# Kernel tuning notes

Hardware: AMD Instinct MI355X
Metric: run time of the kernel (lower is better)

The kernel has to match this reference:

```python
import jax, jax.numpy as jnp
import numpy as np

D_MODEL = 2048
NUM_HEADS = 32
NUM_GROUPS = 8
HEAD_DIM = D_MODEL // NUM_HEADS  # 64
HPG = NUM_HEADS // NUM_GROUPS    # heads per group = 4
B, S = 2, 2048


def setup_inputs() -> dict:
    key = jax.random.key(0)
    ks = jax.random.split(key, 11)
    sd = 1.0 / np.sqrt(D_MODEL)
    kv_dim = HEAD_DIM * NUM_GROUPS
    return {
        "q": jax.random.normal(ks[0], (B, S, D_MODEL), jnp.float32),
        "k": jax.random.normal(ks[1], (B, S, D_MODEL), jnp.float32),
        "v": jax.random.normal(ks[2], (B, S, D_MODEL), jnp.float32),
        "Wq": jax.random.normal(ks[3], (D_MODEL, D_MODEL), jnp.float32) * sd,
        "bq": jnp.zeros((D_MODEL,), jnp.float32),
        "Wk": jax.random.normal(ks[4], (D_MODEL, kv_dim), jnp.float32) * sd,
        "bk": jnp.zeros((kv_dim,), jnp.float32),
        "Wv": jax.random.normal(ks[5], (D_MODEL, kv_dim), jnp.float32) * sd,
        "bv": jnp.zeros((kv_dim,), jnp.float32),
        "Wo": jax.random.normal(ks[6], (D_MODEL, D_MODEL), jnp.float32) * sd,
        "bo": jnp.zeros((D_MODEL,), jnp.float32),
    }


def reference(q, k, v, Wq, bq, Wk, bk, Wv, bv, Wo, bo):
    b, qlen, _ = q.shape
    kvlen = k.shape[1]
    # projections
    qh = (q @ Wq + bq).reshape(b, qlen, NUM_GROUPS, HPG, HEAD_DIM)   # [b,s,g,h,d]
    kh = (k @ Wk + bk).reshape(b, kvlen, NUM_GROUPS, HEAD_DIM)        # [b,t,g,d]
    vh = (v @ Wv + bv).reshape(b, kvlen, NUM_GROUPS, HEAD_DIM)        # [b,t,g,d]
    scale = 1.0 / np.sqrt(HEAD_DIM).astype(np.float32)
    # grouped attention: each group's heads share the same K/V
    scores = jnp.einsum('bsghd,btgd->bghst', qh, kh) * scale          # [b,g,h,s,t]
    attn = jax.nn.softmax(scores, axis=-1)                            # dropout = identity (eval)
    out = jnp.einsum('bghst,btgd->bsghd', attn, vh)                   # [b,s,g,h,d]
    out = out.reshape(b, qlen, D_MODEL)
    return out @ Wo + bo
```

## Files before the change

kernel.cpp:

```cpp
#include <hip/hip_runtime.h>

typedef unsigned short u16;
typedef unsigned int u32;
typedef __attribute__((ext_vector_type(8))) short bf16x8;
typedef __attribute__((ext_vector_type(4))) float f32x4;
typedef __attribute__((ext_vector_type(16))) float f32x16;

#define DM 2048
#define SQ_SCALE (0.125f * 1.44269504089f)

__device__ __forceinline__ u16 f2bf(float f) {
  union { float f; u32 u; } v; v.f = f;
  u32 r = v.u + 0x7fffu + ((v.u >> 16) & 1u);
  return (u16)(r >> 16);
}
__device__ __forceinline__ u32 pkrn(float lo, float hi) {
  union { float f; u32 u; } a, b; a.f = lo; b.f = hi;
  return ((a.u + 0x8000u) >> 16) | ((b.u + 0x8000u) & 0xffff0000u);
}
__device__ __forceinline__ u32 cvtpk(float lo, float hi) {
  u32 r;
  asm("v_cvt_pk_bf16_f32 %0, %1, %2" : "=v"(r) : "v"(lo), "v"(hi));
  return r;
}
__device__ __forceinline__ void gload16(const u16* g, u16* l) {
  __builtin_amdgcn_global_load_lds((const __attribute__((address_space(1))) void*)g,
                                   (__attribute__((address_space(3))) void*)l, 16, 0, 0);
}

__global__ __launch_bounds__(256) void prep(const float* __restrict__ q,
                                            const float* __restrict__ k,
                                            const float* __restrict__ v,
                                            const float* __restrict__ Wq,
                                            const float* __restrict__ Wk,
                                            const float* __restrict__ Wv,
                                            const float* __restrict__ Wo,
                                            u16* __restrict__ qb,
                                            u16* __restrict__ kb,
                                            u16* __restrict__ vb,
                                            u16* __restrict__ WqkvT,
                                            u16* __restrict__ WoT) {
  __shared__ u16 s[64][72];
  int bid = blockIdx.x;
  if (bid < 12288) {
    int z = bid >> 12, x = bid & 4095;
    const float* in = (z == 0) ? q : (z == 1) ? k : v;
    u16* out = (z == 0) ? qb : (z == 1) ? kb : vb;
    size_t i = ((size_t)x * 256 + threadIdx.x) * 8;
    float4 f0 = *(const float4*)(in + i);
    float4 f1 = *(const float4*)(in + i + 4);
    uint4 w = {pkrn(f0.x, f0.y), pkrn(f0.z, f0.w), pkrn(f1.x, f1.y), pkrn(f1.z, f1.w)};
    *(uint4*)(out + i) = w;
    return;
  }
  int off = bid - 12288;
  const float* in; u16* out; int K, N, bx, by;
  if (off < 1024)      { in = Wq; out = WqkvT;                          K = 2048; N = 2048; bx = off & 31; by = off >> 5; }
  else if (off < 1280) { int i2 = off - 1024; in = Wk; out = WqkvT + (size_t)2048 * 2048; K = 2048; N = 512; bx = i2 & 7; by = i2 >> 3; }
  else if (off < 1536) { int i2 = off - 1280; in = Wv; out = WqkvT + (size_t)2560 * 2048; K = 2048; N = 512; bx = i2 & 7; by = i2 >> 3; }
  else                 { int i2 = off - 1536; in = Wo; out = WoT;       K = 2048; N = 2048; bx = i2 & 31; by = i2 >> 5; }
  int n0 = bx * 64, k0 = by * 64;
  int t = threadIdx.x;
  int r = t >> 2;
  int cc = (t & 3) * 16;
  const float* ip = in + (size_t)(k0 + r) * N + n0 + cc;
  u16 tmp[16];
#pragma unroll
  for (int i = 0; i < 16; i += 4) {
    float4 vv = *(const float4*)(ip + i);
    tmp[i] = f2bf(vv.x); tmp[i + 1] = f2bf(vv.y);
    tmp[i + 2] = f2bf(vv.z); tmp[i + 3] = f2bf(vv.w);
  }
  *(uint4*)&s[r][cc] = *(uint4*)tmp;
  *(uint4*)&s[r][cc + 8] = *(uint4*)(tmp + 8);
  __syncthreads();
#pragma unroll
  for (int i = 0; i < 16; i++) tmp[i] = s[cc + i][r];
  u16* op = out + (size_t)(n0 + r) * K + k0 + cc;
  *(uint4*)op = *(uint4*)tmp;
  *(uint4*)(op + 8) = *(uint4*)(tmp + 8);
}

__global__ __launch_bounds__(256) void gemm_proj(const u16* __restrict__ qb,
                                                 const u16* __restrict__ kb,
                                                 const u16* __restrict__ vb,
                                                 const u16* __restrict__ Bt,
                                                 const float* __restrict__ bqp,
                                                 const float* __restrict__ bkp,
                                                 const float* __restrict__ bvp,
                                                 u16* __restrict__ qhb,
                                                 u16* __restrict__ kvb,
                                                 u16* __restrict__ vtb) {
  __shared__ u16 As[2][128 * 32];
  __shared__ u16 Bs[2][128 * 32];
  int n0 = blockIdx.x * 128, m0 = blockIdx.y * 128;
  const u16* A; const float* bias; u16* C; int cw, bofs; float esc;
  if (n0 < 2048)      { A = qb; bias = bqp; C = qhb; cw = 2048; bofs = 0;    esc = SQ_SCALE; }
  else if (n0 < 2560) { A = kb; bias = bkp; C = kvb; cw = 1024; bofs = 2048; esc = 1.0f; }
  else                { A = vb; bias = bvp; C = kvb; cw = 1024; bofs = 2560; esc = 1.0f; }
  int ccol0 = (n0 < 2048) ? n0 : (n0 - 2048);

  int tid = threadIdx.x, wave = tid >> 6, lane = tid & 63;
  int lq = lane & 15, quad = lane >> 4;
  int wm = (wave & 1) * 64, wn = (wave >> 1) * 64;

  f32x4 zero = {0.f, 0.f, 0.f, 0.f};
  f32x4 acc[4][4];
#pragma unroll
  for (int i = 0; i < 4; i++)
#pragma unroll
    for (int j = 0; j < 4; j++) acc[i][j] = zero;

  const u16* gA = A + (size_t)(m0 + wave * 16 + (lane >> 2)) * 2048 + (lane & 3) * 8;
  const u16* gB = Bt + (size_t)(n0 + wave * 16 + (lane >> 2)) * 2048 + (lane & 3) * 8;
  u16* lA0[2] = {&As[0][(wave * 16) * 32], &As[1][(wave * 16) * 32]};
  u16* lA1[2] = {&As[0][(64 + wave * 16) * 32], &As[1][(64 + wave * 16) * 32]};
  u16* lB0[2] = {&Bs[0][(wave * 16) * 32], &Bs[1][(wave * 16) * 32]};
  u16* lB1[2] = {&Bs[0][(64 + wave * 16) * 32], &Bs[1][(64 + wave * 16) * 32]};

  for (int k0 = 0; k0 < 2048; k0 += 64) {
    __syncthreads();
    gload16(gA + k0, lA0[0]);
    gload16(gA + (size_t)64 * 2048 + k0, lA1[0]);
    gload16(gA + k0 + 32, lA0[1]);
    gload16(gA + (size_t)64 * 2048 + k0 + 32, lA1[1]);
    gload16(gB + k0, lB0[0]);
    gload16(gB + (size_t)64 * 2048 + k0, lB1[0]);
    gload16(gB + k0 + 32, lB0[1]);
    gload16(gB + (size_t)64 * 2048 + k0 + 32, lB1[1]);
    __syncthreads();
#pragma unroll
    for (int hf = 0; hf < 2; hf++) {
      bf16x8 af[4], bf[4];
#pragma unroll
      for (int i = 0; i < 4; i++) af[i] = *(const bf16x8*)&As[hf][(wm + i * 16 + lq) * 32 + quad * 8];
#pragma unroll
      for (int j = 0; j < 4; j++) bf[j] = *(const bf16x8*)&Bs[hf][(wn + j * 16 + lq) * 32 + quad * 8];
#pragma unroll
      for (int i = 0; i < 4; i++)
#pragma unroll
        for (int j = 0; j < 4; j++)
          acc[i][j] = __builtin_amdgcn_mfma_f32_16x16x32_bf16(af[i], bf[j], acc[i][j], 0, 0, 0);
    }
  }
  if (n0 >= 2560) {
#pragma unroll
    for (int j = 0; j < 4; j++) {
      int cv = (n0 - 2560) + wn + j * 16 + lq;
      float bvv = bias[cv];
      u16* vout = vtb + (size_t)cv * 2048;
#pragma unroll
      for (int i = 0; i < 4; i++) {
        int row = m0 + wm + i * 16 + quad * 4;
        int bb = row >> 11, tt = row & 2047;
        u16 w4[4];
#pragma unroll
        for (int rg = 0; rg < 4; rg++) w4[rg] = f2bf(acc[i][j][rg] + bvv);
        *(uint2*)(vout + (size_t)bb * 8 * 64 * 2048 + tt) = *(uint2*)w4;
      }
    }
  } else {
#pragma unroll
    for (int j = 0; j < 4; j++) {
      int nglob = n0 + wn + j * 16 + lq;
      float bv = bias[nglob - bofs];
      int col = ccol0 + wn + j * 16 + lq;
#pragma unroll
      for (int i = 0; i < 4; i++) {
#pragma unroll
        for (int rg = 0; rg < 4; rg++) {
          int row = m0 + wm + i * 16 + quad * 4 + rg;
          C[(size_t)row * cw + col] = f2bf((acc[i][j][rg] + bv) * esc);
        }
      }
    }
  }
}

__global__ __launch_bounds__(256) void gemm_o(const u16* __restrict__ A,
                                              const u16* __restrict__ Bt,
                                              const float* __restrict__ bias,
                                              float* __restrict__ C) {
  __shared__ u16 As[2][128 * 32];
  __shared__ u16 Bs[2][128 * 32];
  int n0 = blockIdx.x * 128, m0 = blockIdx.y * 128;
  int tid = threadIdx.x, wave = tid >> 6, lane = tid & 63;
  int lq = lane & 15, quad = lane >> 4;
  int wm = (wave & 1) * 64, wn = (wave >> 1) * 64;

  f32x4 zero = {0.f, 0.f, 0.f, 0.f};
  f32x4 acc[4][4];
#pragma unroll
  for (int i = 0; i < 4; i++)
#pragma unroll
    for (int j = 0; j < 4; j++) acc[i][j] = zero;

  const u16* gA = A + (size_t)(m0 + wave * 16 + (lane >> 2)) * 2048 + (lane & 3) * 8;
  const u16* gB = Bt + (size_t)(n0 + wave * 16 + (lane >> 2)) * 2048 + (lane & 3) * 8;
  u16* lA0[2] = {&As[0][(wave * 16) * 32], &As[1][(wave * 16) * 32]};
  u16* lA1[2] = {&As[0][(64 + wave * 16) * 32], &As[1][(64 + wave * 16) * 32]};
  u16* lB0[2] = {&Bs[0][(wave * 16) * 32], &Bs[1][(wave * 16) * 32]};
  u16* lB1[2] = {&Bs[0][(64 + wave * 16) * 32], &Bs[1][(64 + wave * 16) * 32]};

  for (int k0 = 0; k0 < 2048; k0 += 64) {
    __syncthreads();
    gload16(gA + k0, lA0[0]);
    gload16(gA + (size_t)64 * 2048 + k0, lA1[0]);
    gload16(gA + k0 + 32, lA0[1]);
    gload16(gA + (size_t)64 * 2048 + k0 + 32, lA1[1]);
    gload16(gB + k0, lB0[0]);
    gload16(gB + (size_t)64 * 2048 + k0, lB1[0]);
    gload16(gB + k0 + 32, lB0[1]);
    gload16(gB + (size_t)64 * 2048 + k0 + 32, lB1[1]);
    __syncthreads();
#pragma unroll
    for (int hf = 0; hf < 2; hf++) {
      bf16x8 af[4], bf[4];
#pragma unroll
      for (int i = 0; i < 4; i++) af[i] = *(const bf16x8*)&As[hf][(wm + i * 16 + lq) * 32 + quad * 8];
#pragma unroll
      for (int j = 0; j < 4; j++) bf[j] = *(const bf16x8*)&Bs[hf][(wn + j * 16 + lq) * 32 + quad * 8];
#pragma unroll
      for (int i = 0; i < 4; i++)
#pragma unroll
        for (int j = 0; j < 4; j++)
          acc[i][j] = __builtin_amdgcn_mfma_f32_16x16x32_bf16(af[i], bf[j], acc[i][j], 0, 0, 0);
    }
  }
#pragma unroll
  for (int j = 0; j < 4; j++) {
    int col = n0 + wn + j * 16 + lq;
    float bv = bias[col];
#pragma unroll
    for (int i = 0; i < 4; i++) {
#pragma unroll
      for (int rg = 0; rg < 4; rg++) {
        int row = m0 + wm + i * 16 + quad * 4 + rg;
        C[(size_t)row * 2048 + col] = acc[i][j][rg] + bv;
      }
    }
  }
}

__global__ __launch_bounds__(256) void attn2(const u16* __restrict__ qh,
                                             const u16* __restrict__ kvb,
                                             const u16* __restrict__ vtb,
                                             u16* __restrict__ out) {
  __shared__ u16 Ks[64][72];
  __shared__ u16 Vs[64][72];
  __shared__ float Ls[4][32];
  int flat = blockIdx.x + (blockIdx.y << 4);
  int w = ((flat & 7) << 7) + (flat >> 3);
  int head = w >> 4;
  int b = head >> 5, g = (head >> 2) & 7, h = head & 3;
  int tid = threadIdx.x, wave = tid >> 6, lane = tid & 63;
  int lh = lane & 31, hi = lane >> 5;
  const int qoff = (g * 4 + h) * 64;
  const int koff = g * 64;
  int sBase = (w & 15) * 128 + wave * 32;

  bf16x8 qf[4];
#pragma unroll
  for (int st = 0; st < 4; st++)
    qf[st] = *(const bf16x8*)(qh + (size_t)(b * 2048 + sBase + lh) * DM +
                              qoff + st * 16 + hi * 8);

  f32x16 o_acc[2];
#pragma unroll
  for (int db = 0; db < 2; db++)
#pragma unroll
    for (int r = 0; r < 16; r++) o_acc[db][r] = 0.f;
  float l_acc = 0.f;

  int sr = tid >> 2, sc = (tid & 3) * 16;
  const u16* kbase = kvb + (size_t)b * 2048 * 1024 + koff;
  const u16* vbase = vtb + (size_t)(head >> 2) * 64 * 2048 + (size_t)sr * 2048;

  uint4 kreg0 = *(const uint4*)(kbase + (size_t)sr * 1024 + sc);
  uint4 kreg1 = *(const uint4*)(kbase + (size_t)sr * 1024 + sc + 8);
  uint4 vreg0 = *(const uint4*)(vbase + sc);
  uint4 vreg1 = *(const uint4*)(vbase + sc + 8);

  for (int t0 = 0; t0 < 2048; t0 += 64) {
    __syncthreads();
    *(uint4*)&Ks[sr][sc] = kreg0;
    *(uint4*)&Ks[sr][sc + 8] = kreg1;
    *(uint4*)&Vs[sr][sc] = vreg0;
    *(uint4*)&Vs[sr][sc + 8] = vreg1;
    __syncthreads();
    int tn = (t0 + 64 < 2048) ? t0 + 64 : 0;
    kreg0 = *(const uint4*)(kbase + (size_t)(tn + sr) * 1024 + sc);
    kreg1 = *(const uint4*)(kbase + (size_t)(tn + sr) * 1024 + sc + 8);
    vreg0 = *(const uint4*)(vbase + tn + sc);
    vreg1 = *(const uint4*)(vbase + tn + sc + 8);

#pragma unroll
    for (int u = 0; u < 2; u++) {
      bf16x8 kf[4];
#pragma unroll
      for (int st = 0; st < 4; st++)
        kf[st] = *(const bf16x8*)&Ks[u * 32 + lh][st * 16 + hi * 8];

      f32x16 st_acc;
#pragma unroll
      for (int r = 0; r < 16; r++) st_acc[r] = 0.f;
      __builtin_amdgcn_s_setprio(1);
#pragma unroll
      for (int st = 0; st < 4; st++)
        st_acc = __builtin_amdgcn_mfma_f32_32x32x16_bf16(kf[st], qf[st], st_acc, 0, 0, 0);
      __builtin_amdgcn_s_setprio(0);
      float pr[16];
#pragma unroll
      for (int r = 0; r < 16; r++) pr[r] = __builtin_amdgcn_exp2f(st_acc[r]);
      float s0 = ((pr[0] + pr[1]) + (pr[2] + pr[3])) + ((pr[4] + pr[5]) + (pr[6] + pr[7]));
      float s1 = ((pr[8] + pr[9]) + (pr[10] + pr[11])) + ((pr[12] + pr[13]) + (pr[14] + pr[15]));
      l_acc += s0 + s1;
      u32 pk[8];
#pragma unroll
      for (int a = 0; a < 4; a++) {
        pk[2 * a] = cvtpk(pr[4 * a], pr[4 * a + 1]);
        pk[2 * a + 1] = cvtpk(pr[4 * a + 2], pr[4 * a + 3]);
      }
#pragma unroll
      for (int T2 = 0; T2 < 2; T2++) {
        u32 w0 = pk[4 * T2], w1 = pk[4 * T2 + 1];
        u32 w2 = pk[4 * T2 + 2], w3 = pk[4 * T2 + 3];
        asm("v_permlane32_swap_b32 %0, %1" : "+v"(w0), "+v"(w2));
        asm("v_permlane32_swap_b32 %0, %1" : "+v"(w1), "+v"(w3));
        union { u32 u[4]; bf16x8 v; } af;
        af.u[0] = w0; af.u[1] = w1; af.u[2] = w2; af.u[3] = w3;
        bf16x8 vf[2];
#pragma unroll
        for (int db = 0; db < 2; db++)
          vf[db] = *(const bf16x8*)&Vs[db * 32 + lh][u * 32 + T2 * 16 + hi * 8];
        __builtin_amdgcn_s_setprio(1);
#pragma unroll
        for (int db = 0; db < 2; db++)
          o_acc[db] = __builtin_amdgcn_mfma_f32_32x32x16_bf16(af.v, vf[db], o_acc[db], 0, 0, 0);
        __builtin_amdgcn_s_setprio(0);
      }
    }
  }

  {
    float lt = l_acc + __shfl_xor(l_acc, 32);
    Ls[wave][lh] = 1.0f / lt;
  }
  __builtin_amdgcn_wave_barrier();
  {
    f32x4 inv[4];
#pragma unroll
    for (int a = 0; a < 4; a++) inv[a] = *(const f32x4*)&Ls[wave][8 * a + 4 * hi];
#pragma unroll
    for (int db = 0; db < 2; db++) {
#pragma unroll
      for (int r = 0; r < 16; r++) {
        int srow = (r & 3) + 8 * (r >> 2) + 4 * hi;
        size_t o = (size_t)(b * 2048 + sBase + srow) * DM + qoff + db * 32 + lh;
        out[o] = f2bf(o_acc[db][r] * inv[r >> 2][r & 3]);
      }
    }
  }
}

extern "C" void kernel_launch(void* const* d_in, const int* in_sizes, int n_in,
                              void* d_out, int out_size, void* d_ws, size_t ws_size,
                              hipStream_t stream) {
  const float* q  = (const float*)d_in[0];
  const float* k  = (const float*)d_in[1];
  const float* v  = (const float*)d_in[2];
  const float* Wq = (const float*)d_in[3];
  const float* bq = (const float*)d_in[4];
  const float* Wk = (const float*)d_in[5];
  const float* bk = (const float*)d_in[6];
  const float* Wv = (const float*)d_in[7];
  const float* bv = (const float*)d_in[8];
  const float* Wo = (const float*)d_in[9];
  const float* bo = (const float*)d_in[10];

  u16* p = (u16*)d_ws;
  u16* WqkvT = p; p += (size_t)3072 * 2048;
  u16* WoT   = p; p += (size_t)2048 * 2048;
  u16* qb    = p; p += (size_t)4096 * 2048;
  u16* kb    = p; p += (size_t)4096 * 2048;
  u16* vb    = p; p += (size_t)4096 * 2048;
  u16* qhb   = p; p += (size_t)4096 * 2048;
  u16* kvb   = p; p += (size_t)4096 * 1024;
  u16* vtb   = p; p += (size_t)16 * 64 * 2048;
  u16* att   = qb;

  prep<<<dim3(14848), 256, 0, stream>>>(q, k, v, Wq, Wk, Wv, Wo, qb, kb, vb, WqkvT, WoT);

  gemm_proj<<<dim3(24, 32), 256, 0, stream>>>(qb, kb, vb, WqkvT, bq, bk, bv, qhb, kvb, vtb);

  attn2<<<dim3(16, 64), 256, 0, stream>>>(qhb, kvb, vtb, att);

  gemm_o<<<dim3(16, 32), 256, 0, stream>>>(att, WoT, bo, (float*)d_out);
}
```

Measured before the change: 395.3 us.

## Run attention as single-wave blocks, dropping block-level barriers and shared K/V tiles

Each attention workgroup becomes one 64-lane wave that stages its own 32-key K tile and V tile in LDS, so the kernel no longer needs __syncthreads. The grid becomes 4096 single-wave blocks instead of 1024 four-wave blocks. The aim is to remove barrier stalls and let waves progress independently. In exchange, K/V tiles are no longer shared across four waves, so global/L2 traffic for K and V quadruples per query row. There also appears to be no wave barrier between the LDS writes and reads, which is a correctness risk.

```diff
diff --git a/kernel.cpp b/kernel.cpp
--- a/kernel.cpp
+++ b/kernel.cpp
@@ -242,22 +242,22 @@
   }
 }
 
-__global__ __launch_bounds__(256) void attn2(const u16* __restrict__ qh,
-                                             const u16* __restrict__ kvb,
-                                             const u16* __restrict__ vtb,
-                                             u16* __restrict__ out) {
-  __shared__ u16 Ks[64][72];
-  __shared__ u16 Vs[64][72];
-  __shared__ float Ls[4][32];
-  int flat = blockIdx.x + (blockIdx.y << 4);
-  int w = ((flat & 7) << 7) + (flat >> 3);
-  int head = w >> 4;
+__global__ __launch_bounds__(64) void attn2(const u16* __restrict__ qh,
+                                            const u16* __restrict__ kvb,
+                                            const u16* __restrict__ vtb,
+                                            u16* __restrict__ out) {
+  __shared__ u16 Ks[32][72];
+  __shared__ u16 Vs[64][40];
+  __shared__ float Ls[32];
+  int flat = blockIdx.x;
+  int w = ((flat & 7) << 9) + (flat >> 3);
+  int head = w >> 6;
   int b = head >> 5, g = (head >> 2) & 7, h = head & 3;
-  int tid = threadIdx.x, wave = tid >> 6, lane = tid & 63;
+  int lane = threadIdx.x;
   int lh = lane & 31, hi = lane >> 5;
   const int qoff = (g * 4 + h) * 64;
   const int koff = g * 64;
-  int sBase = (w & 15) * 128 + wave * 32;
+  int sBase = (w & 63) * 32;
 
   bf16x8 qf[4];
 #pragma unroll
@@ -272,85 +272,93 @@
     for (int r = 0; r < 16; r++) o_acc[db][r] = 0.f;
   float l_acc = 0.f;
 
-  int sr = tid >> 2, sc = (tid & 3) * 16;
-  const u16* kbase = kvb + (size_t)b * 2048 * 1024 + koff;
-  const u16* vbase = vtb + (size_t)(head >> 2) * 64 * 2048 + (size_t)sr * 2048;
-
-  uint4 kreg0 = *(const uint4*)(kbase + (size_t)sr * 1024 + sc);
-  uint4 kreg1 = *(const uint4*)(kbase + (size_t)sr * 1024 + sc + 8);
-  uint4 vreg0 = *(const uint4*)(vbase + sc);
-  uint4 vreg1 = *(const uint4*)(vbase + sc + 8);
-
-  for (int t0 = 0; t0 < 2048; t0 += 64) {
-    __syncthreads();
-    *(uint4*)&Ks[sr][sc] = kreg0;
-    *(uint4*)&Ks[sr][sc + 8] = kreg1;
-    *(uint4*)&Vs[sr][sc] = vreg0;
-    *(uint4*)&Vs[sr][sc + 8] = vreg1;
-    __syncthreads();
-    int tn = (t0 + 64 < 2048) ? t0 + 64 : 0;
-    kreg0 = *(const uint4*)(kbase + (size_t)(tn + sr) * 1024 + sc);
-    kreg1 = *(const uint4*)(kbase + (size_t)(tn + sr) * 1024 + sc + 8);
-    vreg0 = *(const uint4*)(vbase + tn + sc);
-    vreg1 = *(const uint4*)(vbase + tn + sc + 8);
-
-#pragma unroll
-    for (int u = 0; u < 2; u++) {
-      bf16x8 kf[4];
-#pragma unroll
-      for (int st = 0; st < 4; st++)
-        kf[st] = *(const bf16x8*)&Ks[u * 32 + lh][st * 16 + hi * 8];
-
-      f32x16 st_acc;
-#pragma unroll
-      for (int r = 0; r < 16; r++) st_acc[r] = 0.f;
+  int sr = lane >> 1, sc = (lane & 1) * 32;
+  const u16* kbase = kvb + (size_t)b * 2048 * 1024 + koff + (size_t)sr * 1024 + sc;
+  const u16* vbase = vtb + (size_t)(head >> 2) * 64 * 2048 + (size_t)lane * 2048;
+
+  uint4 kr[2], vr[2];
+  kr[0] = *(const uint4*)(kbase);
+  kr[1] = *(const uint4*)(kbase + 8);
+  uint4 kr2 = *(const uint4*)(kbase + 16);
+  uint4 kr3 = *(const uint4*)(kbase + 24);
+  vr[0] = *(const uint4*)(vbase);
+  vr[1] = *(const uint4*)(vbase + 8);
+  uint4 vr2 = *(const uint4*)(vbase + 16);
+  uint4 vr3 = *(const uint4*)(vbase + 24);
+
+  for (int t0 = 0; t0 < 2048; t0 += 32) {
+    *(uint4*)&Ks[sr][sc] = kr[0];
+    *(uint4*)&Ks[sr][sc + 8] = kr[1];
+    *(uint4*)&Ks[sr][sc + 16] = kr2;
+    *(uint4*)&Ks[sr][sc + 24] = kr3;
+    *(uint4*)&Vs[lane][0] = vr[0];
+    *(uint4*)&Vs[lane][8] = vr[1];
+    *(uint4*)&Vs[lane][16] = vr2;
+    *(uint4*)&Vs[lane][24] = vr3;
+    int tn = (t0 + 32 < 2048) ? t0 + 32 : 0;
+    kr[0] = *(const uint4*)(kbase + (size_t)tn * 1024);
+    kr[1] = *(const uint4*)(kbase + (size_t)tn * 1024 + 8);
+    kr2 = *(const uint4*)(kbase + (size_t)tn * 1024 + 16);
+    kr3 = *(const uint4*)(kbase + (size_t)tn * 1024 + 24);
+    vr[0] = *(const uint4*)(vbase + tn);
+    vr[1] = *(const uint4*)(vbase + tn + 8);
+    vr2 = *(const uint4*)(vbase + tn + 16);
+    vr3 = *(const uint4*)(vbase + tn + 24);
+
+    bf16x8 kf[4], vf[2][2];
+#pragma unroll
+    for (int st = 0; st < 4; st++) kf[st] = *(const bf16x8*)&Ks[lh][st * 16 + hi * 8];
+#pragma unroll
+    for (int T2 = 0; T2 < 2; T2++)
+#pragma unroll
+      for (int db = 0; db < 2; db++)
+        vf[T2][db] = *(const bf16x8*)&Vs[db * 32 + lh][T2 * 16 + hi * 8];
+
+    f32x16 st_acc;
+#pragma unroll
+    for (int r = 0; r < 16; r++) st_acc[r] = 0.f;
+    __builtin_amdgcn_s_setprio(1);
+#pragma unroll
+    for (int st = 0; st < 4; st++)
+      st_acc = __builtin_amdgcn_mfma_f32_32x32x16_bf16(kf[st], qf[st], st_acc, 0, 0, 0);
+    __builtin_amdgcn_s_setprio(0);
+    float pr[16];
+#pragma unroll
+    for (int r = 0; r < 16; r++) pr[r] = __builtin_amdgcn_exp2f(st_acc[r]);
+    float s0 = ((pr[0] + pr[1]) + (pr[2] + pr[3])) + ((pr[4] + pr[5]) + (pr[6] + pr[7]));
+    float s1 = ((pr[8] + pr[9]) + (pr[10] + pr[11])) + ((pr[12] + pr[13]) + (pr[14] + pr[15]));
+    l_acc += s0 + s1;
+    u32 pk[8];
+#pragma unroll
+    for (int a = 0; a < 4; a++) {
+      pk[2 * a] = cvtpk(pr[4 * a], pr[4 * a + 1]);
+      pk[2 * a + 1] = cvtpk(pr[4 * a + 2], pr[4 * a + 3]);
+    }
+#pragma unroll
+    for (int T2 = 0; T2 < 2; T2++) {
+      u32 w0 = pk[4 * T2], w1 = pk[4 * T2 + 1];
+      u32 w2 = pk[4 * T2 + 2], w3 = pk[4 * T2 + 3];
+      asm("v_permlane32_swap_b32 %0, %1" : "+v"(w0), "+v"(w2));
+      asm("v_permlane32_swap_b32 %0, %1" : "+v"(w1), "+v"(w3));
+      union { u32 u[4]; bf16x8 v; } af;
+      af.u[0] = w0; af.u[1] = w1; af.u[2] = w2; af.u[3] = w3;
       __builtin_amdgcn_s_setprio(1);
 #pragma unroll
-      for (int st = 0; st < 4; st++)
-        st_acc = __builtin_amdgcn_mfma_f32_32x32x16_bf16(kf[st], qf[st], st_acc, 0, 0, 0);
+      for (int db = 0; db < 2; db++)
+        o_acc[db] = __builtin_amdgcn_mfma_f32_32x32x16_bf16(af.v, vf[T2][db], o_acc[db], 0, 0, 0);
       __builtin_amdgcn_s_setprio(0);
-      float pr[16];
-#pragma unroll
-      for (int r = 0; r < 16; r++) pr[r] = __builtin_amdgcn_exp2f(st_acc[r]);
-      float s0 = ((pr[0] + pr[1]) + (pr[2] + pr[3])) + ((pr[4] + pr[5]) + (pr[6] + pr[7]));
-      float s1 = ((pr[8] + pr[9]) + (pr[10] + pr[11])) + ((pr[12] + pr[13]) + (pr[14] + pr[15]));
-      l_acc += s0 + s1;
-      u32 pk[8];
-#pragma unroll
-      for (int a = 0; a < 4; a++) {
-        pk[2 * a] = cvtpk(pr[4 * a], pr[4 * a + 1]);
-        pk[2 * a + 1] = cvtpk(pr[4 * a + 2], pr[4 * a + 3]);
-      }
-#pragma unroll
-      for (int T2 = 0; T2 < 2; T2++) {
-        u32 w0 = pk[4 * T2], w1 = pk[4 * T2 + 1];
-        u32 w2 = pk[4 * T2 + 2], w3 = pk[4 * T2 + 3];
-        asm("v_permlane32_swap_b32 %0, %1" : "+v"(w0), "+v"(w2));
-        asm("v_permlane32_swap_b32 %0, %1" : "+v"(w1), "+v"(w3));
-        union { u32 u[4]; bf16x8 v; } af;
-        af.u[0] = w0; af.u[1] = w1; af.u[2] = w2; af.u[3] = w3;
-        bf16x8 vf[2];
-#pragma unroll
-        for (int db = 0; db < 2; db++)
-          vf[db] = *(const bf16x8*)&Vs[db * 32 + lh][u * 32 + T2 * 16 + hi * 8];
-        __builtin_amdgcn_s_setprio(1);
-#pragma unroll
-        for (int db = 0; db < 2; db++)
-          o_acc[db] = __builtin_amdgcn_mfma_f32_32x32x16_bf16(af.v, vf[db], o_acc[db], 0, 0, 0);
-        __builtin_amdgcn_s_setprio(0);
-      }
     }
   }
 
   {
     float lt = l_acc + __shfl_xor(l_acc, 32);
-    Ls[wave][lh] = 1.0f / lt;
+    Ls[lh] = 1.0f / lt;
   }
   __builtin_amdgcn_wave_barrier();
   {
     f32x4 inv[4];
 #pragma unroll
-    for (int a = 0; a < 4; a++) inv[a] = *(const f32x4*)&Ls[wave][8 * a + 4 * hi];
+    for (int a = 0; a < 4; a++) inv[a] = *(const f32x4*)&Ls[8 * a + 4 * hi];
 #pragma unroll
     for (int db = 0; db < 2; db++) {
 #pragma unroll
@@ -393,7 +401,7 @@
 
   gemm_proj<<<dim3(24, 32), 256, 0, stream>>>(qb, kb, vb, WqkvT, bq, bk, bv, qhb, kvb, vtb);
 
-  attn2<<<dim3(16, 64), 256, 0, stream>>>(qhb, kvb, vtb, att);
+  attn2<<<dim3(4096), 64, 0, stream>>>(qhb, kvb, vtb, att);
 
   gemm_o<<<dim3(16, 32), 256, 0, stream>>>(att, WoT, bo, (float*)d_out);
 }
```

Result: slower. 643.9 us (+62.9%).
